# Performance work log

Measured on AMD Instinct MI355X. Metric: run time of the kernel, lower is better.

Reference implementation:

```python
import jax, jax.numpy as jnp
import numpy as np

NSAMPLE = 64
RADIUS = 0.08
EPS = 1e-5
B, N, M, C = 4, 16384, 1024, 256


def ball_query(xyz, new_xyz, radius, nsample):
    """xyz [B,N,3], new_xyz [B,M,3] -> idx [B,M,nsample] int32.
    Picks first `nsample` points within `radius` of each query (in point order),
    padding with the first found index (0 if none), matching pointnet2 CUDA op."""
    b, n = xyz.shape[0], xyz.shape[1]
    m = new_xyz.shape[1]
    # squared distances via norms + matmul (avoids [B,M,N,3] intermediate)
    d2 = (jnp.sum(new_xyz * new_xyz, -1)[:, :, None]
          + jnp.sum(xyz * xyz, -1)[:, None, :]
          - 2.0 * jnp.einsum('bmc,bnc->bmn', new_xyz, xyz))  # [B,M,N]
    mask = d2 < radius * radius
    rank = jnp.cumsum(mask.astype(jnp.int32), axis=-1) - 1   # slot of each valid point
    valid = mask & (rank < nsample)
    slots = jnp.where(valid, rank, nsample)                  # invalid -> dump slot
    n_idx = jnp.broadcast_to(jnp.arange(n, dtype=jnp.int32), (b, m, n))
    b_idx = jnp.arange(b)[:, None, None]
    m_idx = jnp.arange(m)[None, :, None]
    idx = jnp.zeros((b, m, nsample + 1), jnp.int32)
    idx = idx.at[b_idx, m_idx, slots].set(n_idx)[..., :nsample]
    cnt = jnp.sum(mask, axis=-1)                             # [B,M] neighbors found
    pad = jnp.arange(nsample)[None, None, :] >= cnt[:, :, None]
    idx = jnp.where(pad, idx[:, :, :1], idx)                 # pad with first index
    return idx


def _mlp_layer(x, W, bias, gamma, beta, mu, var):
    # 1x1 conv (pointwise) + BatchNorm (eval, running stats) + ReLU, channels-last
    y = jnp.einsum('bmsc,oc->bmso', x, W) + bias
    y = (y - mu) * (gamma * jax.lax.rsqrt(var + EPS)) + beta
    return jax.nn.relu(y)


def reference(seed_xyz_fps, seed_xyz_graspable, seed_features_graspable,
              W1, b1, g1, be1, m1, v1, W2, b2, g2, be2, m2, v2):
    idx = ball_query(seed_xyz_fps, seed_xyz_graspable, RADIUS, NSAMPLE)  # [B,M,S]
    # gather + relative coordinates (use_xyz=True, normalize_xyz=False)
    gxyz = jax.vmap(lambda p, i: p[i])(seed_xyz_fps, idx)                # [B,M,S,3]
    gxyz = gxyz - seed_xyz_graspable[:, :, None, :]
    feats = jnp.swapaxes(seed_features_graspable, 1, 2)                  # [B,N,C]
    gfeat = jax.vmap(lambda f, i: f[i])(feats, idx)                      # [B,M,S,C]
    x = jnp.concatenate([gxyz, gfeat], axis=-1)                          # [B,M,S,3+C]
    x = _mlp_layer(x, W1, b1, g1, be1, m1, v1)                           # [B,M,S,256]
    x = _mlp_layer(x, W2, b2, g2, be2, m2, v2)                           # [B,M,S,256]
    x = jnp.max(x, axis=2)                                               # [B,M,256]
    return jnp.swapaxes(x, 1, 2)                                         # [B,256,M]


def setup_inputs() -> dict:
    key = jax.random.key(0)
    ks = jax.random.split(key, 16)
    return {
        'seed_xyz_fps': jax.random.uniform(ks[0], (B, N, 3), jnp.float32),
        'seed_xyz_graspable': jax.random.uniform(ks[1], (B, M, 3), jnp.float32),
        'seed_features_graspable': jax.random.normal(ks[2], (B, C, N), jnp.float32),
        'W1': jax.random.normal(ks[3], (256, 3 + C), jnp.float32) * 0.05,
        'b1': jax.random.normal(ks[4], (256,), jnp.float32) * 0.05,
        'g1': jax.random.uniform(ks[5], (256,), jnp.float32, 0.5, 1.5),
        'be1': jax.random.normal(ks[6], (256,), jnp.float32) * 0.05,
        'm1': jax.random.normal(ks[7], (256,), jnp.float32) * 0.1,
        'v1': jax.random.uniform(ks[8], (256,), jnp.float32, 0.5, 1.5),
        'W2': jax.random.normal(ks[9], (256, 256), jnp.float32) * 0.05,
        'b2': jax.random.normal(ks[10], (256,), jnp.float32) * 0.05,
        'g2': jax.random.uniform(ks[11], (256,), jnp.float32, 0.5, 1.5),
        'be2': jax.random.normal(ks[12], (256,), jnp.float32) * 0.05,
        'm2': jax.random.normal(ks[13], (256,), jnp.float32) * 0.1,
        'v2': jax.random.uniform(ks[14], (256,), jnp.float32, 0.5, 1.5),
    }
```

## Files before the change

kernel.cpp:

```cpp
#include <hip/hip_runtime.h>
#include <stdint.h>

typedef __bf16 bf16x8 __attribute__((ext_vector_type(8)));
typedef float f32x4 __attribute__((ext_vector_type(4)));

#define NSAMPLE 64
static constexpr int Bb = 4, Nn = 16384, Mm = 1024, Cc = 256;
static constexpr int K1P = 288;

__device__ __forceinline__ unsigned short f2bf(float f) {
  unsigned int u = __builtin_bit_cast(unsigned int, f);
  u = u + 0x7fffu + ((u >> 16) & 1u);
  return (unsigned short)(u >> 16);
}

__device__ __forceinline__ void gload_lds16(const void* g, void* lds) {
  __builtin_amdgcn_global_load_lds(
      (const __attribute__((address_space(1))) uint32_t*)g,
      (__attribute__((address_space(3))) uint32_t*)lds, 16, 0, 0);
}

__global__ void prep_xyzw_kernel(const float* __restrict__ W1, const float* __restrict__ b1,
                                 const float* __restrict__ g1, const float* __restrict__ be1,
                                 const float* __restrict__ m1, const float* __restrict__ v1,
                                 const float* __restrict__ W2, const float* __restrict__ b2,
                                 const float* __restrict__ g2, const float* __restrict__ be2,
                                 const float* __restrict__ m2, const float* __restrict__ v2,
                                 const float* __restrict__ xyz,
                                 unsigned short* __restrict__ W1b, float* __restrict__ b1e,
                                 unsigned short* __restrict__ W2b, float* __restrict__ b2e,
                                 float4* __restrict__ xyzw) {
  int bx = blockIdx.x;
  if (bx < 288) {
    int t = bx * 256 + threadIdx.x;
    if (t < 256 * K1P) {
      int o = t / K1P, k = t - o * K1P;
      float s = g1[o] / sqrtf(v1[o] + 1e-5f);
      float w = 0.f;
      if (k < 256) w = W1[o * 259 + 3 + k];
      else if (k < 259) w = W1[o * 259 + (k - 256)];
      W1b[t] = f2bf(w * s);
    }
    if (t < 256 * 256) {
      int o = t >> 8;
      float s = g2[o] / sqrtf(v2[o] + 1e-5f);
      W2b[t] = f2bf(W2[t] * s);
    }
    if (t < 256) {
      float s1 = g1[t] / sqrtf(v1[t] + 1e-5f);
      b1e[t] = s1 * (b1[t] - m1[t]) + be1[t];
      float s2 = g2[t] / sqrtf(v2[t] + 1e-5f);
      b2e[t] = s2 * (b2[t] - m2[t]) + be2[t];
    }
    return;
  }
  int t = (bx - 288) * 256 + threadIdx.x;
  float x = xyz[t * 3], y = xyz[t * 3 + 1], z = xyz[t * 3 + 2];
  float pp = __fadd_rn(__fadd_rn(__fmul_rn(x, x), __fmul_rn(y, y)), __fmul_rn(z, z));
  xyzw[t] = make_float4(x, y, z, pp);
}

__global__ void featsT_ballq_kernel(const float* __restrict__ feats,
                                    unsigned short* __restrict__ featsT,
                                    const float4* __restrict__ xyzw,
                                    const float* __restrict__ new_xyz,
                                    int* __restrict__ idx) {
  __shared__ float tile[64][65];
  __shared__ int wl[4][64];
  __shared__ int wcnt[4];
  int bx = blockIdx.x;
  int t = threadIdx.x;
  if (bx < 4096) {
    const float r2 = (float)(0.08 * 0.08);
    int bm = bx;
    int lane = t & 63, w = t >> 6;
    int b = bm >> 10;
    float qx = new_xyz[bm * 3], qy = new_xyz[bm * 3 + 1], qz = new_xyz[bm * 3 + 2];
    float qq = __fadd_rn(__fadd_rn(__fmul_rn(qx, qx), __fmul_rn(qy, qy)), __fmul_rn(qz, qz));
    const float4* P = xyzw + (size_t)b * Nn + w * 4096;
    int cnt = 0;
    for (int n0 = 0; n0 < 4096; n0 += 64) {
      float4 p = P[n0 + lane];
      float dt = __fadd_rn(__fadd_rn(__fmul_rn(qx, p.x), __fmul_rn(qy, p.y)), __fmul_rn(qz, p.z));
      float d2 = __fsub_rn(__fadd_rn(qq, p.w), __fmul_rn(2.f, dt));
      bool valid = d2 < r2;
      unsigned long long mask = __ballot(valid);
      if (mask) {
        if (valid) {
          int pos = cnt + __popcll(mask & ((1ull << lane) - 1ull));
          if (pos < NSAMPLE) wl[w][pos] = w * 4096 + n0 + lane;
        }
        cnt += (int)__popcll(mask);
        if (cnt >= NSAMPLE) break;
      }
    }
    if (lane == 0) wcnt[w] = cnt;
    __syncthreads();
    if (t < NSAMPLE) {
      int c0 = wcnt[0], c1 = wcnt[1], c2 = wcnt[2], c3 = wcnt[3];
      int tot = c0 + c1 + c2 + c3;
      int cc = tot < NSAMPLE ? tot : NSAMPLE;
      int v;
      if (t < cc) {
        if (t < c0) v = wl[0][t];
        else if (t < c0 + c1) v = wl[1][t - c0];
        else if (t < c0 + c1 + c2) v = wl[2][t - c0 - c1];
        else v = wl[3][t - c0 - c1 - c2];
      } else {
        v = (c0 > 0) ? wl[0][0] : (c1 > 0) ? wl[1][0] : (c2 > 0) ? wl[2][0] : (c3 > 0) ? wl[3][0] : 0;
      }
      idx[(size_t)bm * NSAMPLE + t] = v;
    }
    return;
  }
  int fb = bx - 4096;
  int b = fb >> 10;
  int rem = fb & 1023;
  int nt = rem >> 2, ct = rem & 3;
  int tx = t & 63, ty = t >> 6;
  const float* src = feats + ((size_t)b * Cc + ct * 64) * Nn + nt * 64;
#pragma unroll
  for (int i = 0; i < 16; i++) {
    int c = i * 4 + ty;
    tile[c][tx] = src[(size_t)c * Nn + tx];
  }
  __syncthreads();
  unsigned short* dst = featsT + ((size_t)b * Nn + nt * 64) * Cc + ct * 64;
  int c4 = (t & 15) * 4, n0 = t >> 4;
#pragma unroll
  for (int i = 0; i < 4; i++) {
    int n = i * 16 + n0;
    ushort4 v;
    v.x = f2bf(tile[c4][n]);
    v.y = f2bf(tile[c4 + 1][n]);
    v.z = f2bf(tile[c4 + 2][n]);
    v.w = f2bf(tile[c4 + 3][n]);
    *(ushort4*)&dst[(size_t)n * Cc + c4] = v;
  }
}

__global__ __launch_bounds__(256, 4) void fused_kernel(
    const unsigned short* __restrict__ featsT, const float4* __restrict__ xyzw,
    const float* __restrict__ new_xyz, const int* __restrict__ idx,
    const unsigned short* __restrict__ W1b, const float* __restrict__ b1e,
    const unsigned short* __restrict__ W2b, const float* __restrict__ b2e,
    float* __restrict__ out) {
  __shared__ unsigned short Xf[64 * 256];
  __shared__ unsigned short Xco[64 * 40];
  int t = threadIdx.x;
  int wave = t >> 6, lane = t & 63;
  int lr = lane & 15, kg = lane >> 4;
  int wcol = wave * 64;
  int bm = blockIdx.x;
  int b = bm >> 10;

  if (t < 64) {
    int ci = idx[(size_t)bm * NSAMPLE + t];
    float4 p = xyzw[(size_t)b * Nn + ci];
    unsigned int c01 = (unsigned int)f2bf(p.x - new_xyz[bm * 3])
                     | ((unsigned int)f2bf(p.y - new_xyz[bm * 3 + 1]) << 16);
    unsigned int c2 = (unsigned int)f2bf(p.z - new_xyz[bm * 3 + 2]);
    uint4 v0 = make_uint4(c01, c2, 0u, 0u);
    uint4 z = make_uint4(0u, 0u, 0u, 0u);
    uint4* row = (uint4*)&Xco[t * 40];
    row[0] = v0; row[1] = z; row[2] = z; row[3] = z; row[4] = z;
  }
  {
    int idxr = idx[(size_t)bm * NSAMPLE + wave * 16 + (lane & 15)];
#pragma unroll
    for (int i = 0; i < 8; i++) {
      int j = wave * 8 + i;
      int iv = __shfl(idxr, 2 * i + (lane >> 5));
      int r7 = (2 * j + (lane >> 5)) & 7;
      int cg = (lane & 31) ^ r7;
      gload_lds16(featsT + ((size_t)b * Nn + iv) * Cc + cg * 8, &Xf[j * 512]);
    }
  }
  __syncthreads();

  f32x4 acc[4][4];
#pragma unroll
  for (int mi = 0; mi < 4; mi++)
#pragma unroll
    for (int ni = 0; ni < 4; ni++) acc[mi][ni] = (f32x4){0.f, 0.f, 0.f, 0.f};
#pragma unroll
  for (int kk = 0; kk < 9; kk++) {
    bf16x8 w[4];
#pragma unroll
    for (int ni = 0; ni < 4; ni++)
      w[ni] = *(const bf16x8*)&W1b[(size_t)(wcol + ni * 16 + lr) * K1P + kk * 32 + kg * 8];
    bf16x8 a[4];
#pragma unroll
    for (int mi = 0; mi < 4; mi++) {
      int r = mi * 16 + lr;
      if (kk < 8) {
        int cs = ((kk * 4 + kg) ^ (r & 7)) * 8;
        a[mi] = *(const bf16x8*)&Xf[r * 256 + cs];
      } else {
        a[mi] = *(const bf16x8*)&Xco[r * 40 + kg * 8];
      }
    }
    __builtin_amdgcn_s_setprio(1);
#pragma unroll
    for (int mi = 0; mi < 4; mi++)
#pragma unroll
      for (int ni = 0; ni < 4; ni++)
        acc[mi][ni] = __builtin_amdgcn_mfma_f32_16x16x32_bf16(a[mi], w[ni], acc[mi][ni], 0, 0, 0);
    __builtin_amdgcn_s_setprio(0);
  }
  __syncthreads();

#pragma unroll
  for (int ni = 0; ni < 4; ni++) {
    int o = wcol + ni * 16 + lr;
    float bb = b1e[o];
#pragma unroll
    for (int mi = 0; mi < 4; mi++)
#pragma unroll
      for (int j = 0; j < 4; j++) {
        int r = mi * 16 + kg * 4 + j;
        float h = fmaxf(acc[mi][ni][j] + bb, 0.f);
        Xf[r * 256 + ((((o >> 3) ^ (r & 7)) << 3) + (o & 7))] = f2bf(h);
      }
  }
  __syncthreads();

#pragma unroll
  for (int mi = 0; mi < 4; mi++)
#pragma unroll
    for (int ni = 0; ni < 4; ni++) acc[mi][ni] = (f32x4){0.f, 0.f, 0.f, 0.f};
#pragma unroll
  for (int kk = 0; kk < 8; kk++) {
    bf16x8 w[4];
#pragma unroll
    for (int ni = 0; ni < 4; ni++)
      w[ni] = *(const bf16x8*)&W2b[(size_t)(wcol + ni * 16 + lr) * 256 + kk * 32 + kg * 8];
    bf16x8 a[4];
#pragma unroll
    for (int mi = 0; mi < 4; mi++) {
      int r = mi * 16 + lr;
      int cs = ((kk * 4 + kg) ^ (r & 7)) * 8;
      a[mi] = *(const bf16x8*)&Xf[r * 256 + cs];
    }
    __builtin_amdgcn_s_setprio(1);
#pragma unroll
    for (int mi = 0; mi < 4; mi++)
#pragma unroll
      for (int ni = 0; ni < 4; ni++)
        acc[mi][ni] = __builtin_amdgcn_mfma_f32_16x16x32_bf16(a[mi], w[ni], acc[mi][ni], 0, 0, 0);
    __builtin_amdgcn_s_setprio(0);
  }
  {
    int m = bm & (Mm - 1);
#pragma unroll
    for (int ni = 0; ni < 4; ni++) {
      float bv = b2e[wcol + ni * 16 + lr];
      float v = 0.f;
#pragma unroll
      for (int mi = 0; mi < 4; mi++)
#pragma unroll
        for (int j = 0; j < 4; j++) v = fmaxf(v, acc[mi][ni][j] + bv);
      v = fmaxf(v, __shfl_xor(v, 16));
      v = fmaxf(v, __shfl_xor(v, 32));
      if (kg == 0)
        out[((size_t)b * 256 + wcol + ni * 16 + lr) * Mm + m] = v;
    }
  }
}

extern "C" void kernel_launch(void* const* d_in, const int* in_sizes, int n_in,
                              void* d_out, int out_size, void* d_ws, size_t ws_size,
                              hipStream_t stream) {
  (void)in_sizes; (void)n_in; (void)out_size; (void)ws_size;
  const float* xyz     = (const float*)d_in[0];
  const float* new_xyz = (const float*)d_in[1];
  const float* feats   = (const float*)d_in[2];
  const float* W1 = (const float*)d_in[3];
  const float* b1 = (const float*)d_in[4];
  const float* g1 = (const float*)d_in[5];
  const float* be1 = (const float*)d_in[6];
  const float* m1 = (const float*)d_in[7];
  const float* v1 = (const float*)d_in[8];
  const float* W2 = (const float*)d_in[9];
  const float* b2 = (const float*)d_in[10];
  const float* g2 = (const float*)d_in[11];
  const float* be2 = (const float*)d_in[12];
  const float* m2 = (const float*)d_in[13];
  const float* v2 = (const float*)d_in[14];
  float* out = (float*)d_out;

  char* ws = (char*)d_ws;
  unsigned short* W1b   = (unsigned short*)(ws + 0);
  unsigned short* W2b   = (unsigned short*)(ws + 147456);
  float*          b1e   = (float*)(ws + 278528);
  float*          b2e   = (float*)(ws + 279552);
  float4*         xyzw  = (float4*)(ws + 280576);
  unsigned short* featsT= (unsigned short*)(ws + 1329152);
  int*            idx   = (int*)(ws + 34883584);

  prep_xyzw_kernel<<<288 + 256, 256, 0, stream>>>(
      W1, b1, g1, be1, m1, v1, W2, b2, g2, be2, m2, v2, xyz, W1b, b1e, W2b, b2e, xyzw);
  featsT_ballq_kernel<<<4096 + 4096, 256, 0, stream>>>(feats, featsT, xyzw, new_xyz, idx);
  fused_kernel<<<Bb * Mm, 256, 0, stream>>>(featsT, xyzw, new_xyz, idx,
                                            W1b, b1e, W2b, b2e, out);
}
```

Baseline: 175.8 us.

## Process two queries per fused block and move weight prep into ballquery kernel

The fused MLP kernel now handles two query points per 512-thread block. Eight waves split into 2 row groups by 4 column groups, so each weight fragment is fetched by two waves that share a block. The weight/BN folding work moves out of the small first kernel into the ball-query/transpose kernel, leaving only the xyzw computation in the first launch. LDS per block doubles to about 74 KB, which could cut blocks per CU, and __launch_bounds__(512,4) may not be achievable.

```diff
diff --git a/kernel.cpp b/kernel.cpp
--- a/kernel.cpp
+++ b/kernel.cpp
@@ -20,59 +20,56 @@
       (__attribute__((address_space(3))) uint32_t*)lds, 16, 0, 0);
 }
 
-__global__ void prep_xyzw_kernel(const float* __restrict__ W1, const float* __restrict__ b1,
-                                 const float* __restrict__ g1, const float* __restrict__ be1,
-                                 const float* __restrict__ m1, const float* __restrict__ v1,
-                                 const float* __restrict__ W2, const float* __restrict__ b2,
-                                 const float* __restrict__ g2, const float* __restrict__ be2,
-                                 const float* __restrict__ m2, const float* __restrict__ v2,
-                                 const float* __restrict__ xyz,
-                                 unsigned short* __restrict__ W1b, float* __restrict__ b1e,
-                                 unsigned short* __restrict__ W2b, float* __restrict__ b2e,
-                                 float4* __restrict__ xyzw) {
-  int bx = blockIdx.x;
-  if (bx < 288) {
-    int t = bx * 256 + threadIdx.x;
-    if (t < 256 * K1P) {
-      int o = t / K1P, k = t - o * K1P;
-      float s = g1[o] / sqrtf(v1[o] + 1e-5f);
-      float w = 0.f;
-      if (k < 256) w = W1[o * 259 + 3 + k];
-      else if (k < 259) w = W1[o * 259 + (k - 256)];
-      W1b[t] = f2bf(w * s);
-    }
-    if (t < 256 * 256) {
-      int o = t >> 8;
-      float s = g2[o] / sqrtf(v2[o] + 1e-5f);
-      W2b[t] = f2bf(W2[t] * s);
-    }
-    if (t < 256) {
-      float s1 = g1[t] / sqrtf(v1[t] + 1e-5f);
-      b1e[t] = s1 * (b1[t] - m1[t]) + be1[t];
-      float s2 = g2[t] / sqrtf(v2[t] + 1e-5f);
-      b2e[t] = s2 * (b2[t] - m2[t]) + be2[t];
-    }
-    return;
-  }
-  int t = (bx - 288) * 256 + threadIdx.x;
+__global__ void xyzw_kernel(const float* __restrict__ xyz, float4* __restrict__ xyzw) {
+  int t = blockIdx.x * 256 + threadIdx.x;
   float x = xyz[t * 3], y = xyz[t * 3 + 1], z = xyz[t * 3 + 2];
   float pp = __fadd_rn(__fadd_rn(__fmul_rn(x, x), __fmul_rn(y, y)), __fmul_rn(z, z));
   xyzw[t] = make_float4(x, y, z, pp);
 }
 
-__global__ void featsT_ballq_kernel(const float* __restrict__ feats,
-                                    unsigned short* __restrict__ featsT,
-                                    const float4* __restrict__ xyzw,
-                                    const float* __restrict__ new_xyz,
-                                    int* __restrict__ idx) {
+__global__ void prep_featsT_ballq_kernel(
+    const float* __restrict__ W1, const float* __restrict__ b1,
+    const float* __restrict__ g1, const float* __restrict__ be1,
+    const float* __restrict__ m1, const float* __restrict__ v1,
+    const float* __restrict__ W2, const float* __restrict__ b2,
+    const float* __restrict__ g2, const float* __restrict__ be2,
+    const float* __restrict__ m2, const float* __restrict__ v2,
+    unsigned short* __restrict__ W1b, float* __restrict__ b1e,
+    unsigned short* __restrict__ W2b, float* __restrict__ b2e,
+    const float* __restrict__ feats, unsigned short* __restrict__ featsT,
+    const float4* __restrict__ xyzw, const float* __restrict__ new_xyz,
+    int* __restrict__ idx) {
   __shared__ float tile[64][65];
   __shared__ int wl[4][64];
   __shared__ int wcnt[4];
   int bx = blockIdx.x;
   int t = threadIdx.x;
-  if (bx < 4096) {
+  if (bx < 288) {
+    int g = bx * 256 + t;
+    if (g < 256 * K1P) {
+      int o = g / K1P, k = g - o * K1P;
+      float s = g1[o] / sqrtf(v1[o] + 1e-5f);
+      float w = 0.f;
+      if (k < 256) w = W1[o * 259 + 3 + k];
+      else if (k < 259) w = W1[o * 259 + (k - 256)];
+      W1b[g] = f2bf(w * s);
+    }
+    if (g < 256 * 256) {
+      int o = g >> 8;
+      float s = g2[o] / sqrtf(v2[o] + 1e-5f);
+      W2b[g] = f2bf(W2[g] * s);
+    }
+    if (g < 256) {
+      float s1 = g1[g] / sqrtf(v1[g] + 1e-5f);
+      b1e[g] = s1 * (b1[g] - m1[g]) + be1[g];
+      float s2 = g2[g] / sqrtf(v2[g] + 1e-5f);
+      b2e[g] = s2 * (b2[g] - m2[g]) + be2[g];
+    }
+    return;
+  }
+  if (bx < 288 + 4096) {
     const float r2 = (float)(0.08 * 0.08);
-    int bm = bx;
+    int bm = bx - 288;
     int lane = t & 63, w = t >> 6;
     int b = bm >> 10;
     float qx = new_xyz[bm * 3], qy = new_xyz[bm * 3 + 1], qz = new_xyz[bm * 3 + 2];
@@ -113,7 +110,7 @@
     }
     return;
   }
-  int fb = bx - 4096;
+  int fb = bx - (288 + 4096);
   int b = fb >> 10;
   int rem = fb & 1023;
   int nt = rem >> 2, ct = rem & 3;
@@ -139,34 +136,36 @@
   }
 }
 
-__global__ __launch_bounds__(256, 4) void fused_kernel(
+__global__ __launch_bounds__(512, 4) void fused_kernel(
     const unsigned short* __restrict__ featsT, const float4* __restrict__ xyzw,
     const float* __restrict__ new_xyz, const int* __restrict__ idx,
     const unsigned short* __restrict__ W1b, const float* __restrict__ b1e,
     const unsigned short* __restrict__ W2b, const float* __restrict__ b2e,
     float* __restrict__ out) {
-  __shared__ unsigned short Xf[64 * 256];
-  __shared__ unsigned short Xco[64 * 40];
+  __shared__ unsigned short Xf[128 * 256];
+  __shared__ unsigned short Xco[128 * 40];
   int t = threadIdx.x;
   int wave = t >> 6, lane = t & 63;
   int lr = lane & 15, kg = lane >> 4;
-  int wcol = wave * 64;
-  int bm = blockIdx.x;
-  int b = bm >> 10;
-
-  if (t < 64) {
-    int ci = idx[(size_t)bm * NSAMPLE + t];
+  int mg = wave >> 2, ng = wave & 3;
+  int wcol = ng * 64, mrow = mg * 64;
+  int bm0 = blockIdx.x * 2;
+  int b = bm0 >> 10;
+
+  if (t < 128) {
+    int qm = bm0 + (t >> 6);
+    int ci = idx[(size_t)qm * NSAMPLE + (t & 63)];
     float4 p = xyzw[(size_t)b * Nn + ci];
-    unsigned int c01 = (unsigned int)f2bf(p.x - new_xyz[bm * 3])
-                     | ((unsigned int)f2bf(p.y - new_xyz[bm * 3 + 1]) << 16);
-    unsigned int c2 = (unsigned int)f2bf(p.z - new_xyz[bm * 3 + 2]);
+    unsigned int c01 = (unsigned int)f2bf(p.x - new_xyz[qm * 3])
+                     | ((unsigned int)f2bf(p.y - new_xyz[qm * 3 + 1]) << 16);
+    unsigned int c2 = (unsigned int)f2bf(p.z - new_xyz[qm * 3 + 2]);
     uint4 v0 = make_uint4(c01, c2, 0u, 0u);
     uint4 z = make_uint4(0u, 0u, 0u, 0u);
     uint4* row = (uint4*)&Xco[t * 40];
     row[0] = v0; row[1] = z; row[2] = z; row[3] = z; row[4] = z;
   }
   {
-    int idxr = idx[(size_t)bm * NSAMPLE + wave * 16 + (lane & 15)];
+    int idxr = idx[(size_t)(bm0 + (wave >> 2)) * NSAMPLE + (wave & 3) * 16 + (lane & 15)];
 #pragma unroll
     for (int i = 0; i < 8; i++) {
       int j = wave * 8 + i;
@@ -192,7 +191,7 @@
     bf16x8 a[4];
 #pragma unroll
     for (int mi = 0; mi < 4; mi++) {
-      int r = mi * 16 + lr;
+      int r = mrow + mi * 16 + lr;
       if (kk < 8) {
         int cs = ((kk * 4 + kg) ^ (r & 7)) * 8;
         a[mi] = *(const bf16x8*)&Xf[r * 256 + cs];
@@ -218,7 +217,7 @@
     for (int mi = 0; mi < 4; mi++)
 #pragma unroll
       for (int j = 0; j < 4; j++) {
-        int r = mi * 16 + kg * 4 + j;
+        int r = mrow + mi * 16 + kg * 4 + j;
         float h = fmaxf(acc[mi][ni][j] + bb, 0.f);
         Xf[r * 256 + ((((o >> 3) ^ (r & 7)) << 3) + (o & 7))] = f2bf(h);
       }
@@ -238,7 +237,7 @@
     bf16x8 a[4];
 #pragma unroll
     for (int mi = 0; mi < 4; mi++) {
-      int r = mi * 16 + lr;
+      int r = mrow + mi * 16 + lr;
       int cs = ((kk * 4 + kg) ^ (r & 7)) * 8;
       a[mi] = *(const bf16x8*)&Xf[r * 256 + cs];
     }
@@ -251,7 +250,7 @@
     __builtin_amdgcn_s_setprio(0);
   }
   {
-    int m = bm & (Mm - 1);
+    int m = (bm0 + mg) & (Mm - 1);
 #pragma unroll
     for (int ni = 0; ni < 4; ni++) {
       float bv = b2e[wcol + ni * 16 + lr];
@@ -298,9 +297,10 @@
   unsigned short* featsT= (unsigned short*)(ws + 1329152);
   int*            idx   = (int*)(ws + 34883584);
 
-  prep_xyzw_kernel<<<288 + 256, 256, 0, stream>>>(
-      W1, b1, g1, be1, m1, v1, W2, b2, g2, be2, m2, v2, xyz, W1b, b1e, W2b, b2e, xyzw);
-  featsT_ballq_kernel<<<4096 + 4096, 256, 0, stream>>>(feats, featsT, xyzw, new_xyz, idx);
-  fused_kernel<<<Bb * Mm, 256, 0, stream>>>(featsT, xyzw, new_xyz, idx,
-                                            W1b, b1e, W2b, b2e, out);
-}
+  xyzw_kernel<<<(Bb * Nn) / 256, 256, 0, stream>>>(xyz, xyzw);
+  prep_featsT_ballq_kernel<<<288 + 4096 + 4096, 256, 0, stream>>>(
+      W1, b1, g1, be1, m1, v1, W2, b2, g2, be2, m2, v2,
+      W1b, b1e, W2b, b2e, feats, featsT, xyzw, new_xyz, idx);
+  fused_kernel<<<(Bb * Mm) / 2, 512, 0, stream>>>(featsT, xyzw, new_xyz, idx,
+                                                  W1b, b1e, W2b, b2e, out);
+}
```

Result: slower. 186.3 us (+6.0%).
